# Kernel optimization log

Hardware: AMD Instinct MI355X
Metric: run time of the kernel (lower is better)

The kernel has to match this reference:

```python
import jax, jax.numpy as jnp
import numpy as np

N_NODES = 100000
N_EDGES = 3200000
N_GRAPHS = 512
DIM_H = 128
N_LAYERS = 3
N_CLASSES = 10
BN_EPS = 1e-5


def setup_inputs() -> dict:
    key = jax.random.key(0)
    ks = jax.random.split(key, 16)
    s = 1.0 / np.sqrt(DIM_H)
    x = jax.random.normal(ks[0], (N_NODES, DIM_H), dtype=jnp.float32)
    edge_index = jax.random.randint(ks[1], (2, N_EDGES), 0, N_NODES, dtype=jnp.int64)
    batch = jnp.sort(jax.random.randint(ks[2], (N_NODES,), 0, N_GRAPHS, dtype=jnp.int64))
    W1 = jax.random.uniform(ks[3], (N_LAYERS, DIM_H, DIM_H), jnp.float32, -s, s)
    b1 = jax.random.uniform(ks[4], (N_LAYERS, DIM_H), jnp.float32, -s, s)
    gamma = jnp.ones((N_LAYERS, DIM_H), jnp.float32)
    beta = jnp.zeros((N_LAYERS, DIM_H), jnp.float32)
    rmean = 0.1 * jax.random.normal(ks[5], (N_LAYERS, DIM_H), dtype=jnp.float32)
    rvar = jax.random.uniform(ks[6], (N_LAYERS, DIM_H), jnp.float32, 0.5, 1.5)
    W2 = jax.random.uniform(ks[7], (N_LAYERS, DIM_H, DIM_H), jnp.float32, -s, s)
    b2 = jax.random.uniform(ks[8], (N_LAYERS, DIM_H), jnp.float32, -s, s)
    dcat = DIM_H * N_LAYERS
    sf = 1.0 / np.sqrt(dcat)
    Wfin = jax.random.uniform(ks[9], (dcat, dcat), jnp.float32, -sf, sf)
    bfin = jax.random.uniform(ks[10], (dcat,), jnp.float32, -sf, sf)
    Wout = jax.random.uniform(ks[11], (dcat, N_CLASSES), jnp.float32, -sf, sf)
    bout = jax.random.uniform(ks[12], (N_CLASSES,), jnp.float32, -sf, sf)
    return {"x": x, "edge_index": edge_index, "batch": batch, "num_layers": N_LAYERS,
            "W1": W1, "b1": b1, "gamma": gamma, "beta": beta, "rmean": rmean, "rvar": rvar,
            "W2": W2, "b2": b2, "Wfin": Wfin, "bfin": bfin, "Wout": Wout, "bout": bout}


def reference(x, edge_index, batch, num_layers, W1, b1, gamma, beta, rmean, rvar, W2, b2, Wfin, bfin, Wout, bout):
    src, dst = edge_index[0], edge_index[1]
    h = x
    pooled = []
    for i in range(num_layers):
        # GINConv (eps=0): MLP(x + sum_{j in N(i)} x_j)
        aggr = jax.ops.segment_sum(h[src], dst, num_segments=N_NODES)
        z = (h + aggr) @ W1[i] + b1[i]
        # BatchNorm1d in eval mode (running stats)
        z = gamma[i] * (z - rmean[i]) * jax.lax.rsqrt(rvar[i] + BN_EPS) + beta[i]
        z = jax.nn.relu(z)
        h = jax.nn.relu(z @ W2[i] + b2[i])
        # global_add_pool: segment-sum over graph ids
        pooled.append(jax.ops.segment_sum(h, batch, num_segments=N_GRAPHS))
    h_fin = jnp.concatenate(pooled, axis=1)  # [G, dim_h*num_layers]
    h_fin = jax.nn.relu(h_fin @ Wfin + bfin)
    # dropout p=0.5 is identity in eval mode
    logits = h_fin @ Wout + bout
    return logits, jax.nn.log_softmax(logits, axis=1)
```

## Files before the change

### kernel.cpp

```cpp
#include <hip/hip_runtime.h>
#include <stdint.h>

#define N_NODES 100000
#define N_EDGES 3200000
#define N_GRAPHS 512
#define DIM 128
#define M_PAD 100096
#define NGB (M_PAD / 256)
#define NBUCK 391
#define CAP 9216
#define TILE 4096
#define NTILE 782
#define XMM_NB 392

typedef __bf16 bf16x8 __attribute__((ext_vector_type(8)));
typedef float f32x4 __attribute__((ext_vector_type(4)));

__device__ __forceinline__ unsigned short f2bf(float f) {
  unsigned u = __float_as_uint(f);
  u = u + 0x7FFFu + ((u >> 16) & 1u);
  return (unsigned short)(u >> 16);
}
__device__ __forceinline__ float bflo(unsigned v) { return __uint_as_float(v << 16); }
__device__ __forceinline__ float bfhi(unsigned v) { return __uint_as_float(v & 0xFFFF0000u); }
__device__ __forceinline__ float bfs(unsigned short v) { return __uint_as_float(((unsigned)v) << 16); }
__device__ __forceinline__ unsigned packbf(float a, float b) {
  return (unsigned)f2bf(a) | ((unsigned)f2bf(b) << 16);
}

__global__ void k_zero32(int* __restrict__ p, int n) {
  int i = blockIdx.x * 256 + threadIdx.x;
  if (i < n) p[i] = 0;
}

__global__ __launch_bounds__(256) void k_bucket(const int* __restrict__ ei,
                                                int* __restrict__ cnt,
                                                unsigned* __restrict__ rec) {
  __shared__ int hist[NBUCK];
  __shared__ int curs[NBUCK];
  int t = threadIdx.x;
  int base_e = blockIdx.x * TILE;
  int es[16], ed[16];
#pragma unroll
  for (int k = 0; k < 16; ++k) {
    int e = base_e + k * 256 + t;
    if (e < N_EDGES) { es[k] = ei[e]; ed[k] = ei[N_EDGES + e]; }
    else ed[k] = -1;
  }
  for (int i = t; i < NBUCK; i += 256) hist[i] = 0;
  __syncthreads();
#pragma unroll
  for (int k = 0; k < 16; ++k)
    if (ed[k] >= 0) atomicAdd(&hist[ed[k] >> 8], 1);
  __syncthreads();
  for (int i = t; i < NBUCK; i += 256) {
    int h = hist[i];
    int g = h ? atomicAdd(&cnt[i], h) : 0;
    curs[i] = i * CAP + g;
  }
  __syncthreads();
#pragma unroll
  for (int k = 0; k < 16; ++k) {
    if (ed[k] >= 0) {
      int b = ed[k] >> 8;
      int pos = atomicAdd(&curs[b], 1);
      rec[pos] = ((unsigned)es[k] << 8) | (unsigned)(ed[k] & 255);
    }
  }
}

__global__ __launch_bounds__(512) void k_bscan(const int* __restrict__ cnt,
                                               int* __restrict__ bbase,
                                               int* __restrict__ row_ptr) {
  __shared__ int sc[512];
  int t = threadIdx.x;
  int tot = (t < NBUCK) ? min(cnt[t], CAP) : 0;
  sc[t] = tot; __syncthreads();
  for (int off = 1; off < 512; off <<= 1) {
    int x = (t >= off) ? sc[t - off] : 0;
    __syncthreads();
    sc[t] += x;
    __syncthreads();
  }
  if (t < NBUCK) bbase[t] = sc[t] - tot;
  if (t == NBUCK - 1) {
    bbase[NBUCK] = sc[t];
    row_ptr[N_NODES] = sc[t];
  }
}

__global__ __launch_bounds__(256) void k_build(const unsigned* __restrict__ rec,
                                               const int* __restrict__ cnt,
                                               const int* __restrict__ bbase,
                                               int* __restrict__ row_ptr,
                                               int* __restrict__ col) {
  __shared__ int hist[256];
  __shared__ int sc[256];
  __shared__ int curs[256];
  int b = blockIdx.x, t = threadIdx.x;
  int n = min(cnt[b], CAP);
  const unsigned* p = rec + (size_t)b * CAP;
  hist[t] = 0; __syncthreads();
  for (int i = t; i < n; i += 256) atomicAdd(&hist[p[i] & 255u], 1);
  __syncthreads();
  int v = hist[t];
  sc[t] = v; __syncthreads();
  for (int off = 1; off < 256; off <<= 1) {
    int x = (t >= off) ? sc[t - off] : 0;
    __syncthreads();
    sc[t] += x;
    __syncthreads();
  }
  int excl = bbase[b] + sc[t] - v;
  int node = (b << 8) + t;
  if (node < N_NODES) row_ptr[node] = excl;
  curs[t] = excl;
  __syncthreads();
  for (int i = t; i < n; i += 256) {
    unsigned w = p[i];
    int pos = atomicAdd(&curs[w & 255u], 1);
    col[pos] = (int)(w >> 8);
  }
}

__global__ __launch_bounds__(256) void k_xmm1(const float* __restrict__ x,
                                              float* __restrict__ pmax,
                                              float* __restrict__ pmin) {
  __shared__ float smx[8][32][4];
  __shared__ float smn[8][32][4];
  int t = threadIdx.x;
  int c4 = t & 31;
  int ro = t >> 5;
  float mx0 = 0.f, mx1 = 0.f, mx2 = 0.f, mx3 = 0.f;
  float mn0 = 0.f, mn1 = 0.f, mn2 = 0.f, mn3 = 0.f;
  for (int row = blockIdx.x * 8 + ro; row < N_NODES; row += XMM_NB * 8) {
    float4 v = ((const float4*)x)[(size_t)row * 32 + c4];
    mx0 = fmaxf(mx0, v.x); mn0 = fmaxf(mn0, -v.x);
    mx1 = fmaxf(mx1, v.y); mn1 = fmaxf(mn1, -v.y);
    mx2 = fmaxf(mx2, v.z); mn2 = fmaxf(mn2, -v.z);
    mx3 = fmaxf(mx3, v.w); mn3 = fmaxf(mn3, -v.w);
  }
  smx[ro][c4][0] = mx0; smx[ro][c4][1] = mx1; smx[ro][c4][2] = mx2; smx[ro][c4][3] = mx3;
  smn[ro][c4][0] = mn0; smn[ro][c4][1] = mn1; smn[ro][c4][2] = mn2; smn[ro][c4][3] = mn3;
  __syncthreads();
  for (int off = 4; off > 0; off >>= 1) {
    if (ro < off) {
#pragma unroll
      for (int k = 0; k < 4; ++k) {
        smx[ro][c4][k] = fmaxf(smx[ro][c4][k], smx[ro + off][c4][k]);
        smn[ro][c4][k] = fmaxf(smn[ro][c4][k], smn[ro + off][c4][k]);
      }
    }
    __syncthreads();
  }
  if (ro == 0) {
#pragma unroll
    for (int k = 0; k < 4; ++k) {
      pmax[blockIdx.x * 128 + c4 * 4 + k] = smx[0][c4][k];
      pmin[blockIdx.x * 128 + c4 * 4 + k] = smn[0][c4][k];
    }
  }
}

__global__ __launch_bounds__(64) void k_xmm2(const float* __restrict__ pmax,
                                             const float* __restrict__ pmin,
                                             float* __restrict__ xmx,
                                             float* __restrict__ xminf) {
  int c = blockIdx.x & 127;
  int isMin = blockIdx.x >> 7;
  const float* src = isMin ? pmin : pmax;
  int l = threadIdx.x;
  float m = 0.f;
  for (int p2 = l; p2 < XMM_NB; p2 += 64) m = fmaxf(m, src[p2 * 128 + c]);
#pragma unroll
  for (int off = 32; off > 0; off >>= 1) m = fmaxf(m, __shfl_down(m, off));
  if (l == 0) {
    if (isMin) xminf[c] = -m;
    else xmx[c] = m;
  }
}

__global__ __launch_bounds__(64) void k_hred(const float* __restrict__ pmaxb,
                                             float* __restrict__ hmax) {
  int c = blockIdx.x;
  float m = 0.f;
  for (int b = threadIdx.x; b < NGB; b += 64) m = fmaxf(m, pmaxb[(size_t)b * 128 + c]);
#pragma unroll
  for (int off = 32; off > 0; off >>= 1) m = fmaxf(m, __shfl_down(m, off));
  if (threadIdx.x == 0) hmax[c] = m;
}

__global__ void k_convx(const float* __restrict__ x, const float* __restrict__ qmin,
                        const float* __restrict__ qmax, unsigned short* __restrict__ xq) {
  int i = blockIdx.x * 256 + threadIdx.x;
  if (i >= M_PAD * 64) return;
  int lane = i & 63;
  unsigned short o = 0;
  if ((i >> 6) < N_NODES) {
    float mn0 = qmin[2 * lane], mn1 = qmin[2 * lane + 1];
    float r0 = qmax[2 * lane] - mn0, r1 = qmax[2 * lane + 1] - mn1;
    float is0 = r0 > 1e-20f ? 255.f / r0 : 0.f;
    float is1 = r1 > 1e-20f ? 255.f / r1 : 0.f;
    float2 f = ((const float2*)x)[i];
    int q0 = (int)rintf((f.x - mn0) * is0); q0 = min(max(q0, 0), 255);
    int q1 = (int)rintf((f.y - mn1) * is1); q1 = min(max(q1, 0), 255);
    o = (unsigned short)(q0 | (q1 << 8));
  }
  xq[i] = o;
}

__global__ void k_quant(const unsigned* __restrict__ hbf, const float* __restrict__ qmax,
                        unsigned short* __restrict__ hq) {
  int i = blockIdx.x * 256 + threadIdx.x;
  if (i >= M_PAD * 64) return;
  if ((i >> 6) >= N_NODES) { hq[i] = 0; return; }
  int lane = i & 63;
  float mx0 = qmax[2 * lane], mx1 = qmax[2 * lane + 1];
  float is0 = mx0 > 1e-20f ? 255.f / mx0 : 0.f;
  float is1 = mx1 > 1e-20f ? 255.f / mx1 : 0.f;
  unsigned v = hbf[i];
  int q0 = (int)rintf(bflo(v) * is0); q0 = min(max(q0, 0), 255);
  int q1 = (int)rintf(bfhi(v) * is1); q1 = min(max(q1, 0), 255);
  hq[i] = (unsigned short)(q0 | (q1 << 8));
}

__global__ void k_convw(const float* __restrict__ W1, const float* __restrict__ W2,
                        unsigned short* __restrict__ Wt1, unsigned short* __restrict__ Wt2) {
  int i = blockIdx.x * 256 + threadIdx.x;
  if (i >= 3 * DIM * DIM) return;
  int l = i >> 14, rem = i & 16383, k = rem >> 7, n = rem & 127;
  int o = (l << 14) + (n << 7) + k;
  Wt1[o] = f2bf(W1[i]);
  Wt2[o] = f2bf(W2[i]);
}

__global__ void k_coef(const float* __restrict__ b1, const float* __restrict__ gamma,
                       const float* __restrict__ beta, const float* __restrict__ rmean,
                       const float* __restrict__ rvar, const float* __restrict__ b2,
                       float* __restrict__ sA1, float* __restrict__ sB1,
                       float* __restrict__ sA2, float* __restrict__ sB2) {
  int i = blockIdx.x * 128 + threadIdx.x;
  if (i >= 3 * DIM) return;
  float sa = gamma[i] * rsqrtf(rvar[i] + 1e-5f);
  sA1[i] = sa;
  sB1[i] = fmaf(sa, b1[i] - rmean[i], beta[i]);
  sA2[i] = 1.0f;
  sB2[i] = b2[i];
}

__global__ __launch_bounds__(256) void k_aggr(const unsigned short* __restrict__ hq,
                                              const int* __restrict__ row_ptr,
                                              const int* __restrict__ col,
                                              const float* __restrict__ qmin,
                                              const float* __restrict__ qmax,
                                              unsigned* __restrict__ tmp) {
  const uint4* hq128 = (const uint4*)hq;
  const unsigned* hq32 = (const unsigned*)hq;
  int wv = (blockIdx.x << 2) + (threadIdx.x >> 6);
  int lane = threadIdx.x & 63;
  int grp = lane >> 3;
  int lo8 = lane & 7;
  int dw = lane & 31;
  if (wv >= M_PAD) return;
  if (wv >= N_NODES) {
    ((uint2*)(tmp + (size_t)wv * 64))[dw] = make_uint2(0u, 0u);
    return;
  }
  unsigned ae0 = 0, ae1 = 0, ae2 = 0, ae3 = 0;
  unsigned ao0 = 0, ao1 = 0, ao2 = 0, ao3 = 0;
  int s = __builtin_amdgcn_readfirstlane(row_ptr[wv]);
  int e = __builtin_amdgcn_readfirstlane(row_ptr[wv + 1]);
  int pidx = (lo8 << 3) + grp;
  for (int base = s; base < e; base += 32) {
    int n = e - base; if (n > 32) n = 32;
    int cv = (pidx < n) ? col[base + pidx] : 0;
    int s0 = __builtin_amdgcn_ds_swizzle(cv, 0x18);
    int s1 = __builtin_amdgcn_ds_swizzle(cv, 0x38);
    int s2 = __builtin_amdgcn_ds_swizzle(cv, 0x58);
    int s3 = __builtin_amdgcn_ds_swizzle(cv, 0x78);
    s0 = (grp      < n) ? s0 : N_NODES;
    s1 = (grp +  8 < n) ? s1 : N_NODES;
    s2 = (grp + 16 < n) ? s2 : N_NODES;
    s3 = (grp + 24 < n) ? s3 : N_NODES;
    uint4 v0 = hq128[s0 * 8 + lo8];
    uint4 v1 = hq128[s1 * 8 + lo8];
    uint4 v2 = hq128[s2 * 8 + lo8];
    uint4 v3 = hq128[s3 * 8 + lo8];
    ae0 += v0.x & 0x00FF00FFu; ao0 += (v0.x >> 8) & 0x00FF00FFu;
    ae1 += v0.y & 0x00FF00FFu; ao1 += (v0.y >> 8) & 0x00FF00FFu;
    ae2 += v0.z & 0x00FF00FFu; ao2 += (v0.z >> 8) & 0x00FF00FFu;
    ae3 += v0.w & 0x00FF00FFu; ao3 += (v0.w >> 8) & 0x00FF00FFu;
    ae0 += v1.x & 0x00FF00FFu; ao0 += (v1.x >> 8) & 0x00FF00FFu;
    ae1 += v1.y & 0x00FF00FFu; ao1 += (v1.y >> 8) & 0x00FF00FFu;
    ae2 += v1.z & 0x00FF00FFu; ao2 += (v1.z >> 8) & 0x00FF00FFu;
    ae3 += v1.w & 0x00FF00FFu; ao3 += (v1.w >> 8) & 0x00FF00FFu;
    ae0 += v2.x & 0x00FF00FFu; ao0 += (v2.x >> 8) & 0x00FF00FFu;
    ae1 += v2.y & 0x00FF00FFu; ao1 += (v2.y >> 8) & 0x00FF00FFu;
    ae2 += v2.z & 0x00FF00FFu; ao2 += (v2.z >> 8) & 0x00FF00FFu;
    ae3 += v2.w & 0x00FF00FFu; ao3 += (v2.w >> 8) & 0x00FF00FFu;
    ae0 += v3.x & 0x00FF00FFu; ao0 += (v3.x >> 8) & 0x00FF00FFu;
    ae1 += v3.y & 0x00FF00FFu; ao1 += (v3.y >> 8) & 0x00FF00FFu;
    ae2 += v3.z & 0x00FF00FFu; ao2 += (v3.z >> 8) & 0x00FF00FFu;
    ae3 += v3.w & 0x00FF00FFu; ao3 += (v3.w >> 8) & 0x00FF00FFu;
  }
  ae0 += __shfl_xor(ae0, 8); ae0 += __shfl_xor(ae0, 16); ae0 += __shfl_xor(ae0, 32);
  ae1 += __shfl_xor(ae1, 8); ae1 += __shfl_xor(ae1, 16); ae1 += __shfl_xor(ae1, 32);
  ae2 += __shfl_xor(ae2, 8); ae2 += __shfl_xor(ae2, 16); ae2 += __shfl_xor(ae2, 32);
  ae3 += __shfl_xor(ae3, 8); ae3 += __shfl_xor(ae3, 16); ae3 += __shfl_xor(ae3, 32);
  ao0 += __shfl_xor(ao0, 8); ao0 += __shfl_xor(ao0, 16); ao0 += __shfl_xor(ao0, 32);
  ao1 += __shfl_xor(ao1, 8); ao1 += __shfl_xor(ao1, 16); ao1 += __shfl_xor(ao1, 32);
  ao2 += __shfl_xor(ao2, 8); ao2 += __shfl_xor(ao2, 16); ao2 += __shfl_xor(ao2, 32);
  ao3 += __shfl_xor(ao3, 8); ao3 += __shfl_xor(ao3, 16); ao3 += __shfl_xor(ao3, 32);
  {
    int ba = ((dw >> 2) & 7) << 2;
    unsigned f0 = (unsigned)__builtin_amdgcn_ds_bpermute(ba, (int)ae0);
    unsigned f1 = (unsigned)__builtin_amdgcn_ds_bpermute(ba, (int)ae1);
    unsigned f2 = (unsigned)__builtin_amdgcn_ds_bpermute(ba, (int)ae2);
    unsigned f3 = (unsigned)__builtin_amdgcn_ds_bpermute(ba, (int)ae3);
    unsigned g0 = (unsigned)__builtin_amdgcn_ds_bpermute(ba, (int)ao0);
    unsigned g1 = (unsigned)__builtin_amdgcn_ds_bpermute(ba, (int)ao1);
    unsigned g2 = (unsigned)__builtin_amdgcn_ds_bpermute(ba, (int)ao2);
    unsigned g3 = (unsigned)__builtin_amdgcn_ds_bpermute(ba, (int)ao3);
    unsigned el = (dw & 1) ? f1 : f0;
    unsigned eh = (dw & 1) ? f3 : f2;
    unsigned ae = (dw & 2) ? eh : el;
    unsigned ol = (dw & 1) ? g1 : g0;
    unsigned oh = (dw & 1) ? g3 : g2;
    unsigned ao = (dw & 2) ? oh : ol;
    if (lane < 32) {
      unsigned v = hq32[wv * 32 + dw];
      ae += v & 0x00FF00FFu;
      ao += (v >> 8) & 0x00FF00FFu;
      float cntf = (float)(e - s + 1);
      float4 qn = ((const float4*)qmin)[dw];
      float4 qx = ((const float4*)qmax)[dw];
      const float k255 = 1.0f / 255.0f;
      float A0 = fmaf(qn.x, cntf, (qx.x - qn.x) * k255 * (float)(ae & 0xFFFFu));
      float A1 = fmaf(qn.y, cntf, (qx.y - qn.y) * k255 * (float)(ao & 0xFFFFu));
      float A2 = fmaf(qn.z, cntf, (qx.z - qn.z) * k255 * (float)(ae >> 16));
      float A3 = fmaf(qn.w, cntf, (qx.w - qn.w) * k255 * (float)(ao >> 16));
      ((uint2*)(tmp + (size_t)wv * 64))[dw] = make_uint2(packbf(A0, A1), packbf(A2, A3));
    }
  }
}

__global__ __launch_bounds__(256, 2) void k_gemm12(const unsigned short* __restrict__ A,
                                                   const unsigned short* __restrict__ Wt1,
                                                   const float* __restrict__ sA1,
                                                   const float* __restrict__ sB1,
                                                   const unsigned short* __restrict__ Wt2,
                                                   const float* __restrict__ sA2,
                                                   const float* __restrict__ sB2,
                                                   const int* __restrict__ batch,
                                                   unsigned short* __restrict__ out,
                                                   float* __restrict__ pooled8, int layer,
                                                   float* __restrict__ pmaxb, int do_max) {
  __shared__ unsigned short zt[4][64][136];
  __shared__ float colred[128];
  __shared__ int sgid[256];
  int w = threadIdx.x >> 6, lane = threadIdx.x & 63;
  int q = lane >> 4, n16 = lane & 15;
  int rbase = (blockIdx.x << 8) + (w << 6);
  if (do_max && threadIdx.x < 128) colred[threadIdx.x] = 0.f;
  {
    int rr = (blockIdx.x << 8) + threadIdx.x;
    sgid[threadIdx.x] = (rr < N_NODES) ? batch[rr] : -1;
  }

  {
    bf16x8 Bf[4][8];
#pragma unroll
    for (int ks = 0; ks < 4; ++ks)
#pragma unroll
      for (int c = 0; c < 8; ++c)
        Bf[ks][c] = *(const bf16x8*)(Wt1 + (size_t)((c << 4) + n16) * DIM + ks * 32 + q * 8);
#pragma unroll
    for (int t = 0; t < 4; ++t) {
      int r0 = rbase + (t << 4);
      f32x4 acc[8] = {};
#pragma unroll
      for (int ks = 0; ks < 4; ++ks) {
        bf16x8 a = *(const bf16x8*)(A + (size_t)(r0 + n16) * DIM + ks * 32 + q * 8);
#pragma unroll
        for (int c = 0; c < 8; ++c)
          acc[c] = __builtin_amdgcn_mfma_f32_16x16x32_bf16(a, Bf[ks][c], acc[c], 0, 0, 0);
      }
#pragma unroll
      for (int c = 0; c < 8; ++c) {
        int colc = (c << 4) + n16;
        float s = sA1[colc], tt = sB1[colc];
#pragma unroll
        for (int r = 0; r < 4; ++r) {
          float v = fmaxf(fmaf(s, acc[c][r], tt), 0.0f);
          zt[w][(t << 4) + (q << 2) + r][colc] = f2bf(v);
        }
      }
    }
  }

  float mcol[8];
#pragma unroll
  for (int c = 0; c < 8; ++c) mcol[c] = 0.f;
  {
    bf16x8 Bf[4][8];
#pragma unroll
    for (int ks = 0; ks < 4; ++ks)
#pragma unroll
      for (int c = 0; c < 8; ++c)
        Bf[ks][c] = *(const bf16x8*)(Wt2 + (size_t)((c << 4) + n16) * DIM + ks * 32 + q * 8);
#pragma unroll
    for (int t = 0; t < 4; ++t) {
      int r0 = rbase + (t << 4);
      f32x4 acc[8] = {};
#pragma unroll
      for (int ks = 0; ks < 4; ++ks) {
        bf16x8 a = *(const bf16x8*)(&zt[w][(t << 4) + n16][ks * 32 + q * 8]);
#pragma unroll
        for (int c = 0; c < 8; ++c)
          acc[c] = __builtin_amdgcn_mfma_f32_16x16x32_bf16(a, Bf[ks][c], acc[c], 0, 0, 0);
      }
      __builtin_amdgcn_s_waitcnt(0);
#pragma unroll
      for (int c = 0; c < 8; ++c) {
        int colc = (c << 4) + n16;
        float s = sA2[colc], tt = sB2[colc];
#pragma unroll
        for (int r = 0; r < 4; ++r) {
          float v = fmaxf(fmaf(s, acc[c][r], tt), 0.0f);
          mcol[c] = fmaxf(mcol[c], v);
          unsigned short hv = f2bf(v);
          out[(size_t)(r0 + (q << 2) + r) * DIM + colc] = hv;
          zt[w][(t << 4) + (q << 2) + r][colc] = hv;
        }
      }
    }
  }
  __syncthreads();

  {
    const unsigned short* ztf = &zt[0][0][0];
    int colp = threadIdx.x & 127, grp = threadIdx.x >> 7;
    int cp = blockIdx.x & 7;
    float pacc = 0.f;
    int gcur = sgid[grp << 7];
    for (int r = 0; r < 128; ++r) {
      int row = (grp << 7) + r;
      int g = sgid[row];
      if (g != gcur) {
        if (gcur >= 0)
          atomicAdd(&pooled8[((size_t)cp * N_GRAPHS + gcur) * 384 + layer * DIM + colp], pacc);
        pacc = 0.f; gcur = g;
      }
      if (g >= 0) pacc += bfs(ztf[row * 136 + colp]);
    }
    if (gcur >= 0)
      atomicAdd(&pooled8[((size_t)cp * N_GRAPHS + gcur) * 384 + layer * DIM + colp], pacc);
  }

  if (do_max) {
#pragma unroll
    for (int c = 0; c < 8; ++c)
      atomicMax((int*)&colred[(c << 4) + n16], __float_as_int(mcol[c]));
    __syncthreads();
    if (threadIdx.x < 128)
      pmaxb[(size_t)blockIdx.x * 128 + threadIdx.x] = colred[threadIdx.x];
  }
}

__global__ __launch_bounds__(384) void k_head(const float* __restrict__ pooled8,
                                              const float* __restrict__ Wfin,
                                              const float* __restrict__ bfin,
                                              const float* __restrict__ Wout,
                                              const float* __restrict__ bout,
                                              float* __restrict__ out) {
  __shared__ float p[8][384];
  __shared__ float hf[8][392];
  __shared__ float lg[8][10];
  __shared__ float lse[8];
  int t = threadIdx.x, g0 = blockIdx.x << 3;
  for (int i = t; i < 8 * 384; i += 384) {
    int gl = i / 384, k = i % 384;
    float s = 0.f;
#pragma unroll
    for (int cp = 0; cp < 8; ++cp)
      s += pooled8[((size_t)cp * N_GRAPHS + g0 + gl) * 384 + k];
    p[gl][k] = s;
  }
  __syncthreads();
  float bb = bfin[t];
  float acc[8];
#pragma unroll
  for (int g = 0; g < 8; ++g) acc[g] = bb;
  for (int k = 0; k < 384; ++k) {
    float wv = Wfin[k * 384 + t];
#pragma unroll
    for (int g = 0; g < 8; ++g) acc[g] = fmaf(p[g][k], wv, acc[g]);
  }
#pragma unroll
  for (int g = 0; g < 8; ++g) hf[g][t] = fmaxf(acc[g], 0.f);
  __syncthreads();
  if (t < 80) {
    int g = t / 10, c = t % 10;
    float a = bout[c];
    for (int k = 0; k < 384; ++k) a = fmaf(hf[g][k], Wout[k * 10 + c], a);
    lg[g][c] = a;
  }
  __syncthreads();
  if (t < 8) {
    float m = lg[t][0];
#pragma unroll
    for (int i = 1; i < 10; ++i) m = fmaxf(m, lg[t][i]);
    float ss = 0.f;
#pragma unroll
    for (int i = 0; i < 10; ++i) ss += __expf(lg[t][i] - m);
    lse[t] = m + __logf(ss);
  }
  __syncthreads();
  if (t < 80) {
    int g = t / 10, c = t % 10;
    out[(size_t)(g0 + g) * 10 + c] = lg[g][c];
    out[(size_t)N_GRAPHS * 10 + (size_t)(g0 + g) * 10 + c] = lg[g][c] - lse[g];
  }
}

extern "C" void kernel_launch(void* const* d_in, const int* in_sizes, int n_in,
                              void* d_out, int out_size, void* d_ws, size_t ws_size,
                              hipStream_t stream) {
  const float* x     = (const float*)d_in[0];
  const int*   ei    = (const int*)d_in[1];
  const int*   batch = (const int*)d_in[2];
  const float* W1    = (const float*)d_in[4];
  const float* b1    = (const float*)d_in[5];
  const float* gamma = (const float*)d_in[6];
  const float* beta  = (const float*)d_in[7];
  const float* rmean = (const float*)d_in[8];
  const float* rvar  = (const float*)d_in[9];
  const float* W2    = (const float*)d_in[10];
  const float* b2    = (const float*)d_in[11];
  const float* Wfin  = (const float*)d_in[12];
  const float* bfin  = (const float*)d_in[13];
  const float* Wout  = (const float*)d_in[14];
  const float* bout  = (const float*)d_in[15];
  float* out = (float*)d_out;

  char* p = (char*)d_ws;
  auto alloc = [&](size_t bytes) { char* r = p; p += (bytes + 255) & ~255ull; return r; };
  int* cnt      = (int*)alloc(NBUCK * 4);
  unsigned* rec = (unsigned*)alloc((size_t)NBUCK * CAP * 4);
  int* bbase    = (int*)alloc((NBUCK + 1) * 4);
  int* row_ptr  = (int*)alloc((N_NODES + 1) * 4);
  int* colb     = (int*)alloc((size_t)N_EDGES * 4);
  unsigned short* xq  = (unsigned short*)alloc((size_t)M_PAD * 64 * 2);
  unsigned short* hqb = (unsigned short*)alloc((size_t)M_PAD * 64 * 2);
  unsigned* hbf  = (unsigned*)alloc((size_t)M_PAD * 64 * 4);
  unsigned* tmpb = (unsigned*)alloc((size_t)M_PAD * 64 * 4);
  unsigned short* Wt1 = (unsigned short*)alloc(3 * DIM * DIM * 2);
  unsigned short* Wt2 = (unsigned short*)alloc(3 * DIM * DIM * 2);
  float* pmax   = (float*)alloc((size_t)XMM_NB * 128 * 4);
  float* pmin   = (float*)alloc((size_t)XMM_NB * 128 * 4);
  float* pmaxb  = (float*)alloc((size_t)NGB * 128 * 4);
  float* sA1    = (float*)alloc(384 * 4);
  float* sB1    = (float*)alloc(384 * 4);
  float* sA2    = (float*)alloc(384 * 4);
  float* sB2    = (float*)alloc(384 * 4);
  float* qbuf   = (float*)alloc(1024 * 4);
  float* xmx    = qbuf + 128;
  float* xminf  = qbuf + 256;
  float* hmax0  = qbuf + 384;
  float* hmax1  = qbuf + 512;
  float* zeros  = qbuf + 640;
  float* pooled8 = (float*)alloc((size_t)8 * N_GRAPHS * 384 * 4);

  k_zero32<<<(NBUCK + 255) / 256, 256, 0, stream>>>(cnt, NBUCK);
  k_zero32<<<4, 256, 0, stream>>>((int*)qbuf, 1024);
  k_zero32<<<(8 * N_GRAPHS * 384 + 255) / 256, 256, 0, stream>>>((int*)pooled8, 8 * N_GRAPHS * 384);

  k_bucket<<<NTILE, 256, 0, stream>>>(ei, cnt, rec);
  k_bscan<<<1, 512, 0, stream>>>(cnt, bbase, row_ptr);
  k_build<<<NBUCK, 256, 0, stream>>>(rec, cnt, bbase, row_ptr, colb);

  k_xmm1<<<XMM_NB, 256, 0, stream>>>(x, pmax, pmin);
  k_xmm2<<<256, 64, 0, stream>>>(pmax, pmin, xmx, xminf);
  k_convx<<<(M_PAD * 64 + 255) / 256, 256, 0, stream>>>(x, xminf, xmx, xq);
  k_convw<<<(3 * DIM * DIM + 255) / 256, 256, 0, stream>>>(W1, W2, Wt1, Wt2);
  k_coef<<<3, 128, 0, stream>>>(b1, gamma, beta, rmean, rvar, b2, sA1, sB1, sA2, sB2);

  k_aggr<<<M_PAD / 4, 256, 0, stream>>>(xq, row_ptr, colb, xminf, xmx, tmpb);
  k_gemm12<<<NGB, 256, 0, stream>>>((const unsigned short*)tmpb, Wt1, sA1, sB1,
                                    Wt2, sA2, sB2, batch, (unsigned short*)hbf,
                                    pooled8, 0, pmaxb, 1);
  k_hred<<<128, 64, 0, stream>>>(pmaxb, hmax0);
  k_quant<<<(M_PAD * 64 + 255) / 256, 256, 0, stream>>>(hbf, hmax0, hqb);
  k_aggr<<<M_PAD / 4, 256, 0, stream>>>(hqb, row_ptr, colb, zeros, hmax0, tmpb);
  k_gemm12<<<NGB, 256, 0, stream>>>((const unsigned short*)tmpb, Wt1 + DIM * DIM,
                                    sA1 + DIM, sB1 + DIM, Wt2 + DIM * DIM,
                                    sA2 + DIM, sB2 + DIM, batch, (unsigned short*)hbf,
                                    pooled8, 1, pmaxb, 1);
  k_hred<<<128, 64, 0, stream>>>(pmaxb, hmax1);
  k_quant<<<(M_PAD * 64 + 255) / 256, 256, 0, stream>>>(hbf, hmax1, hqb);
  k_aggr<<<M_PAD / 4, 256, 0, stream>>>(hqb, row_ptr, colb, zeros, hmax1, tmpb);
  k_gemm12<<<NGB, 256, 0, stream>>>((const unsigned short*)tmpb, Wt1 + 2 * DIM * DIM,
                                    sA1 + 2 * DIM, sB1 + 2 * DIM, Wt2 + 2 * DIM * DIM,
                                    sA2 + 2 * DIM, sB2 + 2 * DIM, batch, (unsigned short*)hbf,
                                    pooled8, 2, pmaxb, 0);

  k_head<<<N_GRAPHS / 8, 384, 0, stream>>>(pooled8, Wfin, bfin, Wout, bout, out);
}
```

Before: 621.1 us.

## Process two nodes per wavefront in aggregation with batched gathers

```diff
diff --git a/kernel.cpp b/kernel.cpp
--- a/kernel.cpp
+++ b/kernel.cpp
@@ -248,6 +248,63 @@
   sB2[i] = b2[i];
 }
 
+#define SWZ(cv, J) __builtin_amdgcn_ds_swizzle((cv), (0x18 | ((J) << 5)))
+
+__device__ __forceinline__ void acc8(const uint4& v, unsigned& e0, unsigned& e1,
+                                     unsigned& e2, unsigned& e3, unsigned& o0,
+                                     unsigned& o1, unsigned& o2, unsigned& o3) {
+  e0 += v.x & 0x00FF00FFu; o0 += (v.x >> 8) & 0x00FF00FFu;
+  e1 += v.y & 0x00FF00FFu; o1 += (v.y >> 8) & 0x00FF00FFu;
+  e2 += v.z & 0x00FF00FFu; o2 += (v.z >> 8) & 0x00FF00FFu;
+  e3 += v.w & 0x00FF00FFu; o3 += (v.w >> 8) & 0x00FF00FFu;
+}
+
+__device__ __forceinline__ void epi_store(unsigned ae0, unsigned ae1, unsigned ae2, unsigned ae3,
+                                          unsigned ao0, unsigned ao1, unsigned ao2, unsigned ao3,
+                                          int wv, int s, int e, int lane, int dw,
+                                          const unsigned* __restrict__ hq32,
+                                          const float* __restrict__ qmin,
+                                          const float* __restrict__ qmax,
+                                          unsigned* __restrict__ tmp) {
+  ae0 += __shfl_xor(ae0, 8); ae0 += __shfl_xor(ae0, 16); ae0 += __shfl_xor(ae0, 32);
+  ae1 += __shfl_xor(ae1, 8); ae1 += __shfl_xor(ae1, 16); ae1 += __shfl_xor(ae1, 32);
+  ae2 += __shfl_xor(ae2, 8); ae2 += __shfl_xor(ae2, 16); ae2 += __shfl_xor(ae2, 32);
+  ae3 += __shfl_xor(ae3, 8); ae3 += __shfl_xor(ae3, 16); ae3 += __shfl_xor(ae3, 32);
+  ao0 += __shfl_xor(ao0, 8); ao0 += __shfl_xor(ao0, 16); ao0 += __shfl_xor(ao0, 32);
+  ao1 += __shfl_xor(ao1, 8); ao1 += __shfl_xor(ao1, 16); ao1 += __shfl_xor(ao1, 32);
+  ao2 += __shfl_xor(ao2, 8); ao2 += __shfl_xor(ao2, 16); ao2 += __shfl_xor(ao2, 32);
+  ao3 += __shfl_xor(ao3, 8); ao3 += __shfl_xor(ao3, 16); ao3 += __shfl_xor(ao3, 32);
+  int ba = ((dw >> 2) & 7) << 2;
+  unsigned f0 = (unsigned)__builtin_amdgcn_ds_bpermute(ba, (int)ae0);
+  unsigned f1 = (unsigned)__builtin_amdgcn_ds_bpermute(ba, (int)ae1);
+  unsigned f2 = (unsigned)__builtin_amdgcn_ds_bpermute(ba, (int)ae2);
+  unsigned f3 = (unsigned)__builtin_amdgcn_ds_bpermute(ba, (int)ae3);
+  unsigned g0 = (unsigned)__builtin_amdgcn_ds_bpermute(ba, (int)ao0);
+  unsigned g1 = (unsigned)__builtin_amdgcn_ds_bpermute(ba, (int)ao1);
+  unsigned g2 = (unsigned)__builtin_amdgcn_ds_bpermute(ba, (int)ao2);
+  unsigned g3 = (unsigned)__builtin_amdgcn_ds_bpermute(ba, (int)ao3);
+  unsigned el = (dw & 1) ? f1 : f0;
+  unsigned eh = (dw & 1) ? f3 : f2;
+  unsigned ae = (dw & 2) ? eh : el;
+  unsigned ol = (dw & 1) ? g1 : g0;
+  unsigned oh = (dw & 1) ? g3 : g2;
+  unsigned ao = (dw & 2) ? oh : ol;
+  if (lane < 32) {
+    unsigned v = hq32[wv * 32 + dw];
+    ae += v & 0x00FF00FFu;
+    ao += (v >> 8) & 0x00FF00FFu;
+    float cntf = (float)(e - s + 1);
+    float4 qn = ((const float4*)qmin)[dw];
+    float4 qx = ((const float4*)qmax)[dw];
+    const float k255 = 1.0f / 255.0f;
+    float A0 = fmaf(qn.x, cntf, (qx.x - qn.x) * k255 * (float)(ae & 0xFFFFu));
+    float A1 = fmaf(qn.y, cntf, (qx.y - qn.y) * k255 * (float)(ao & 0xFFFFu));
+    float A2 = fmaf(qn.z, cntf, (qx.z - qn.z) * k255 * (float)(ae >> 16));
+    float A3 = fmaf(qn.w, cntf, (qx.w - qn.w) * k255 * (float)(ao >> 16));
+    ((uint2*)(tmp + (size_t)wv * 64))[dw] = make_uint2(packbf(A0, A1), packbf(A2, A3));
+  }
+}
+
 __global__ __launch_bounds__(256) void k_aggr(const unsigned short* __restrict__ hq,
                                               const int* __restrict__ row_ptr,
                                               const int* __restrict__ col,
@@ -256,92 +313,125 @@
                                               unsigned* __restrict__ tmp) {
   const uint4* hq128 = (const uint4*)hq;
   const unsigned* hq32 = (const unsigned*)hq;
-  int wv = (blockIdx.x << 2) + (threadIdx.x >> 6);
+  int wid = (blockIdx.x << 2) + (threadIdx.x >> 6);
+  int wv0 = wid << 1, wv1 = wv0 + 1;
   int lane = threadIdx.x & 63;
   int grp = lane >> 3;
   int lo8 = lane & 7;
   int dw = lane & 31;
-  if (wv >= M_PAD) return;
-  if (wv >= N_NODES) {
-    ((uint2*)(tmp + (size_t)wv * 64))[dw] = make_uint2(0u, 0u);
+  if (wv0 >= M_PAD) return;
+  if (wv0 >= N_NODES) {
+    ((uint2*)(tmp + (size_t)wv0 * 64))[dw] = make_uint2(0u, 0u);
+    if (wv1 < M_PAD) ((uint2*)(tmp + (size_t)wv1 * 64))[dw] = make_uint2(0u, 0u);
     return;
   }
-  unsigned ae0 = 0, ae1 = 0, ae2 = 0, ae3 = 0;
-  unsigned ao0 = 0, ao1 = 0, ao2 = 0, ao3 = 0;
-  int s = __builtin_amdgcn_readfirstlane(row_ptr[wv]);
-  int e = __builtin_amdgcn_readfirstlane(row_ptr[wv + 1]);
+  int s0 = __builtin_amdgcn_readfirstlane(row_ptr[wv0]);
+  int mB = __builtin_amdgcn_readfirstlane(row_ptr[wv0 + 1]);
+  int e1 = __builtin_amdgcn_readfirstlane(row_ptr[wv0 + 2]);
+  int nA = mB - s0; if (nA > 64) nA = 64;
+  int nB = e1 - mB; if (nB > 64) nB = 64;
   int pidx = (lo8 << 3) + grp;
-  for (int base = s; base < e; base += 32) {
-    int n = e - base; if (n > 32) n = 32;
+  int cvA = (pidx < nA) ? col[s0 + pidx] : 0;
+  int cvB = (pidx < nB) ? col[mB + pidx] : 0;
+
+  unsigned ae0 = 0, ae1 = 0, ae2 = 0, ae3 = 0, ao0 = 0, ao1 = 0, ao2 = 0, ao3 = 0;
+  unsigned be0 = 0, be1 = 0, be2 = 0, be3 = 0, bo0 = 0, bo1 = 0, bo2 = 0, bo3 = 0;
+
+  int a0 = SWZ(cvA, 0); a0 = (grp      < nA) ? a0 : N_NODES;
+  int a1 = SWZ(cvA, 1); a1 = (grp +  8 < nA) ? a1 : N_NODES;
+  int a2 = SWZ(cvA, 2); a2 = (grp + 16 < nA) ? a2 : N_NODES;
+  int a3 = SWZ(cvA, 3); a3 = (grp + 24 < nA) ? a3 : N_NODES;
+  uint4 vA0 = hq128[(size_t)a0 * 8 + lo8];
+  uint4 vA1 = hq128[(size_t)a1 * 8 + lo8];
+  uint4 vA2 = hq128[(size_t)a2 * 8 + lo8];
+  uint4 vA3 = hq128[(size_t)a3 * 8 + lo8];
+  int b0 = SWZ(cvB, 0); b0 = (grp      < nB) ? b0 : N_NODES;
+  int b1 = SWZ(cvB, 1); b1 = (grp +  8 < nB) ? b1 : N_NODES;
+  int b2 = SWZ(cvB, 2); b2 = (grp + 16 < nB) ? b2 : N_NODES;
+  int b3 = SWZ(cvB, 3); b3 = (grp + 24 < nB) ? b3 : N_NODES;
+  uint4 vB0 = hq128[(size_t)b0 * 8 + lo8];
+  uint4 vB1 = hq128[(size_t)b1 * 8 + lo8];
+  uint4 vB2 = hq128[(size_t)b2 * 8 + lo8];
+  uint4 vB3 = hq128[(size_t)b3 * 8 + lo8];
+
+  bool hA = nA > 32, hB = nB > 32;
+  uint4 vA4, vA5, vA6, vA7, vB4, vB5, vB6, vB7;
+  if (hA) {
+    int a4 = SWZ(cvA, 4); a4 = (grp + 32 < nA) ? a4 : N_NODES;
+    int a5 = SWZ(cvA, 5); a5 = (grp + 40 < nA) ? a5 : N_NODES;
+    int a6 = SWZ(cvA, 6); a6 = (grp + 48 < nA) ? a6 : N_NODES;
+    int a7 = SWZ(cvA, 7); a7 = (grp + 56 < nA) ? a7 : N_NODES;
+    vA4 = hq128[(size_t)a4 * 8 + lo8];
+    vA5 = hq128[(size_t)a5 * 8 + lo8];
+    vA6 = hq128[(size_t)a6 * 8 + lo8];
+    vA7 = hq128[(size_t)a7 * 8 + lo8];
+  }
+  acc8(vA0, ae0, ae1, ae2, ae3, ao0, ao1, ao2, ao3);
+  acc8(vA1, ae0, ae1, ae2, ae3, ao0, ao1, ao2, ao3);
+  acc8(vA2, ae0, ae1, ae2, ae3, ao0, ao1, ao2, ao3);
+  acc8(vA3, ae0, ae1, ae2, ae3, ao0, ao1, ao2, ao3);
+  if (hB) {
+    int b4 = SWZ(cvB, 4); b4 = (grp + 32 < nB) ? b4 : N_NODES;
+    int b5 = SWZ(cvB, 5); b5 = (grp + 40 < nB) ? b5 : N_NODES;
+    int b6 = SWZ(cvB, 6); b6 = (grp + 48 < nB) ? b6 : N_NODES;
+    int b7 = SWZ(cvB, 7); b7 = (grp + 56 < nB) ? b7 : N_NODES;
+    vB4 = hq128[(size_t)b4 * 8 + lo8];
+    vB5 = hq128[(size_t)b5 * 8 + lo8];
+    vB6 = hq128[(size_t)b6 * 8 + lo8];
+    vB7 = hq128[(size_t)b7 * 8 + lo8];
+  }
+  acc8(vB0, be0, be1, be2, be3, bo0, bo1, bo2, bo3);
+  acc8(vB1, be0, be1, be2, be3, bo0, bo1, bo2, bo3);
+  acc8(vB2, be0, be1, be2, be3, bo0, bo1, bo2, bo3);
+  acc8(vB3, be0, be1, be2, be3, bo0, bo1, bo2, bo3);
+  if (hA) {
+    acc8(vA4, ae0, ae1, ae2, ae3, ao0, ao1, ao2, ao3);
+    acc8(vA5, ae0, ae1, ae2, ae3, ao0, ao1, ao2, ao3);
+    acc8(vA6, ae0, ae1, ae2, ae3, ao0, ao1, ao2, ao3);
+    acc8(vA7, ae0, ae1, ae2, ae3, ao0, ao1, ao2, ao3);
+  }
+  if (hB) {
+    acc8(vB4, be0, be1, be2, be3, bo0, bo1, bo2, bo3);
+    acc8(vB5, be0, be1, be2, be3, bo0, bo1, bo2, bo3);
+    acc8(vB6, be0, be1, be2, be3, bo0, bo1, bo2, bo3);
+    acc8(vB7, be0, be1, be2, be3, bo0, bo1, bo2, bo3);
+  }
+
+  for (int base = s0 + 64; base < mB; base += 32) {
+    int n = mB - base; if (n > 32) n = 32;
     int cv = (pidx < n) ? col[base + pidx] : 0;
-    int s0 = __builtin_amdgcn_ds_swizzle(cv, 0x18);
-    int s1 = __builtin_amdgcn_ds_swizzle(cv, 0x38);
-    int s2 = __builtin_amdgcn_ds_swizzle(cv, 0x58);
-    int s3 = __builtin_amdgcn_ds_swizzle(cv, 0x78);
-    s0 = (grp      < n) ? s0 : N_NODES;
-    s1 = (grp +  8 < n) ? s1 : N_NODES;
-    s2 = (grp + 16 < n) ? s2 : N_NODES;
-    s3 = (grp + 24 < n) ? s3 : N_NODES;
-    uint4 v0 = hq128[s0 * 8 + lo8];
-    uint4 v1 = hq128[s1 * 8 + lo8];
-    uint4 v2 = hq128[s2 * 8 + lo8];
-    uint4 v3 = hq128[s3 * 8 + lo8];
-    ae0 += v0.x & 0x00FF00FFu; ao0 += (v0.x >> 8) & 0x00FF00FFu;
-    ae1 += v0.y & 0x00FF00FFu; ao1 += (v0.y >> 8) & 0x00FF00FFu;
-    ae2 += v0.z & 0x00FF00FFu; ao2 += (v0.z >> 8) & 0x00FF00FFu;
-    ae3 += v0.w & 0x00FF00FFu; ao3 += (v0.w >> 8) & 0x00FF00FFu;
-    ae0 += v1.x & 0x00FF00FFu; ao0 += (v1.x >> 8) & 0x00FF00FFu;
-    ae1 += v1.y & 0x00FF00FFu; ao1 += (v1.y >> 8) & 0x00FF00FFu;
-    ae2 += v1.z & 0x00FF00FFu; ao2 += (v1.z >> 8) & 0x00FF00FFu;
-    ae3 += v1.w & 0x00FF00FFu; ao3 += (v1.w >> 8) & 0x00FF00FFu;
-    ae0 += v2.x & 0x00FF00FFu; ao0 += (v2.x >> 8) & 0x00FF00FFu;
-    ae1 += v2.y & 0x00FF00FFu; ao1 += (v2.y >> 8) & 0x00FF00FFu;
-    ae2 += v2.z & 0x00FF00FFu; ao2 += (v2.z >> 8) & 0x00FF00FFu;
-    ae3 += v2.w & 0x00FF00FFu; ao3 += (v2.w >> 8) & 0x00FF00FFu;
-    ae0 += v3.x & 0x00FF00FFu; ao0 += (v3.x >> 8) & 0x00FF00FFu;
-    ae1 += v3.y & 0x00FF00FFu; ao1 += (v3.y >> 8) & 0x00FF00FFu;
-    ae2 += v3.z & 0x00FF00FFu; ao2 += (v3.z >> 8) & 0x00FF00FFu;
-    ae3 += v3.w & 0x00FF00FFu; ao3 += (v3.w >> 8) & 0x00FF00FFu;
-  }
-  ae0 += __shfl_xor(ae0, 8); ae0 += __shfl_xor(ae0, 16); ae0 += __shfl_xor(ae0, 32);
-  ae1 += __shfl_xor(ae1, 8); ae1 += __shfl_xor(ae1, 16); ae1 += __shfl_xor(ae1, 32);
-  ae2 += __shfl_xor(ae2, 8); ae2 += __shfl_xor(ae2, 16); ae2 += __shfl_xor(ae2, 32);
-  ae3 += __shfl_xor(ae3, 8); ae3 += __shfl_xor(ae3, 16); ae3 += __shfl_xor(ae3, 32);
-  ao0 += __shfl_xor(ao0, 8); ao0 += __shfl_xor(ao0, 16); ao0 += __shfl_xor(ao0, 32);
-  ao1 += __shfl_xor(ao1, 8); ao1 += __shfl_xor(ao1, 16); ao1 += __shfl_xor(ao1, 32);
-  ao2 += __shfl_xor(ao2, 8); ao2 += __shfl_xor(ao2, 16); ao2 += __shfl_xor(ao2, 32);
-  ao3 += __shfl_xor(ao3, 8); ao3 += __shfl_xor(ao3, 16); ao3 += __shfl_xor(ao3, 32);
-  {
-    int ba = ((dw >> 2) & 7) << 2;
-    unsigned f0 = (unsigned)__builtin_amdgcn_ds_bpermute(ba, (int)ae0);
-    unsigned f1 = (unsigned)__builtin_amdgcn_ds_bpermute(ba, (int)ae1);
-    unsigned f2 = (unsigned)__builtin_amdgcn_ds_bpermute(ba, (int)ae2);
-    unsigned f3 = (unsigned)__builtin_amdgcn_ds_bpermute(ba, (int)ae3);
-    unsigned g0 = (unsigned)__builtin_amdgcn_ds_bpermute(ba, (int)ao0);
-    unsigned g1 = (unsigned)__builtin_amdgcn_ds_bpermute(ba, (int)ao1);
-    unsigned g2 = (unsigned)__builtin_amdgcn_ds_bpermute(ba, (int)ao2);
-    unsigned g3 = (unsigned)__builtin_amdgcn_ds_bpermute(ba, (int)ao3);
-    unsigned el = (dw & 1) ? f1 : f0;
-    unsigned eh = (dw & 1) ? f3 : f2;
-    unsigned ae = (dw & 2) ? eh : el;
-    unsigned ol = (dw & 1) ? g1 : g0;
-    unsigned oh = (dw & 1) ? g3 : g2;
-    unsigned ao = (dw & 2) ? oh : ol;
-    if (lane < 32) {
-      unsigned v = hq32[wv * 32 + dw];
-      ae += v & 0x00FF00FFu;
-      ao += (v >> 8) & 0x00FF00FFu;
-      float cntf = (float)(e - s + 1);
-      float4 qn = ((const float4*)qmin)[dw];
-      float4 qx = ((const float4*)qmax)[dw];
-      const float k255 = 1.0f / 255.0f;
-      float A0 = fmaf(qn.x, cntf, (qx.x - qn.x) * k255 * (float)(ae & 0xFFFFu));
-      float A1 = fmaf(qn.y, cntf, (qx.y - qn.y) * k255 * (float)(ao & 0xFFFFu));
-      float A2 = fmaf(qn.z, cntf, (qx.z - qn.z) * k255 * (float)(ae >> 16));
-      float A3 = fmaf(qn.w, cntf, (qx.w - qn.w) * k255 * (float)(ao >> 16));
-      ((uint2*)(tmp + (size_t)wv * 64))[dw] = make_uint2(packbf(A0, A1), packbf(A2, A3));
-    }
-  }
+    int t0 = SWZ(cv, 0); t0 = (grp      < n) ? t0 : N_NODES;
+    int t1 = SWZ(cv, 1); t1 = (grp +  8 < n) ? t1 : N_NODES;
+    int t2 = SWZ(cv, 2); t2 = (grp + 16 < n) ? t2 : N_NODES;
+    int t3 = SWZ(cv, 3); t3 = (grp + 24 < n) ? t3 : N_NODES;
+    uint4 u0 = hq128[(size_t)t0 * 8 + lo8];
+    uint4 u1 = hq128[(size_t)t1 * 8 + lo8];
+    uint4 u2 = hq128[(size_t)t2 * 8 + lo8];
+    uint4 u3 = hq128[(size_t)t3 * 8 + lo8];
+    acc8(u0, ae0, ae1, ae2, ae3, ao0, ao1, ao2, ao3);
+    acc8(u1, ae0, ae1, ae2, ae3, ao0, ao1, ao2, ao3);
+    acc8(u2, ae0, ae1, ae2, ae3, ao0, ao1, ao2, ao3);
+    acc8(u3, ae0, ae1, ae2, ae3, ao0, ao1, ao2, ao3);
+  }
+  for (int base = mB + 64; base < e1; base += 32) {
+    int n = e1 - base; if (n > 32) n = 32;
+    int cv = (pidx < n) ? col[base + pidx] : 0;
+    int t0 = SWZ(cv, 0); t0 = (grp      < n) ? t0 : N_NODES;
+    int t1 = SWZ(cv, 1); t1 = (grp +  8 < n) ? t1 : N_NODES;
+    int t2 = SWZ(cv, 2); t2 = (grp + 16 < n) ? t2 : N_NODES;
+    int t3 = SWZ(cv, 3); t3 = (grp + 24 < n) ? t3 : N_NODES;
+    uint4 u0 = hq128[(size_t)t0 * 8 + lo8];
+    uint4 u1 = hq128[(size_t)t1 * 8 + lo8];
+    uint4 u2 = hq128[(size_t)t2 * 8 + lo8];
+    uint4 u3 = hq128[(size_t)t3 * 8 + lo8];
+    acc8(u0, be0, be1, be2, be3, bo0, bo1, bo2, bo3);
+    acc8(u1, be0, be1, be2, be3, bo0, bo1, bo2, bo3);
+    acc8(u2, be0, be1, be2, be3, bo0, bo1, bo2, bo3);
+    acc8(u3, be0, be1, be2, be3, bo0, bo1, bo2, bo3);
+  }
+
+  epi_store(ae0, ae1, ae2, ae3, ao0, ao1, ao2, ao3, wv0, s0, mB, lane, dw, hq32, qmin, qmax, tmp);
+  epi_store(be0, be1, be2, be3, bo0, bo1, bo2, bo3, wv1, mB, e1, lane, dw, hq32, qmin, qmax, tmp);
 }
 
 __global__ __launch_bounds__(256, 2) void k_gemm12(const unsigned short* __restrict__ A,
@@ -585,20 +675,20 @@
   k_convw<<<(3 * DIM * DIM + 255) / 256, 256, 0, stream>>>(W1, W2, Wt1, Wt2);
   k_coef<<<3, 128, 0, stream>>>(b1, gamma, beta, rmean, rvar, b2, sA1, sB1, sA2, sB2);
 
-  k_aggr<<<M_PAD / 4, 256, 0, stream>>>(xq, row_ptr, colb, xminf, xmx, tmpb);
+  k_aggr<<<M_PAD / 8, 256, 0, stream>>>(xq, row_ptr, colb, xminf, xmx, tmpb);
   k_gemm12<<<NGB, 256, 0, stream>>>((const unsigned short*)tmpb, Wt1, sA1, sB1,
                                     Wt2, sA2, sB2, batch, (unsigned short*)hbf,
                                     pooled8, 0, pmaxb, 1);
   k_hred<<<128, 64, 0, stream>>>(pmaxb, hmax0);
   k_quant<<<(M_PAD * 64 + 255) / 256, 256, 0, stream>>>(hbf, hmax0, hqb);
-  k_aggr<<<M_PAD / 4, 256, 0, stream>>>(hqb, row_ptr, colb, zeros, hmax0, tmpb);
+  k_aggr<<<M_PAD / 8, 256, 0, stream>>>(hqb, row_ptr, colb, zeros, hmax0, tmpb);
   k_gemm12<<<NGB, 256, 0, stream>>>((const unsigned short*)tmpb, Wt1 + DIM * DIM,
                                     sA1 + DIM, sB1 + DIM, Wt2 + DIM * DIM,
                                     sA2 + DIM, sB2 + DIM, batch, (unsigned short*)hbf,
                                     pooled8, 1, pmaxb, 1);
   k_hred<<<128, 64, 0, stream>>>(pmaxb, hmax1);
   k_quant<<<(M_PAD * 64 + 255) / 256, 256, 0, stream>>>(hbf, hmax1, hqb);
-  k_aggr<<<M_PAD / 4, 256, 0, stream>>>(hqb, row_ptr, colb, zeros, hmax1, tmpb);
+  k_aggr<<<M_PAD / 8, 256, 0, stream>>>(hqb, row_ptr, colb, zeros, hmax1, tmpb);
   k_gemm12<<<NGB, 256, 0, stream>>>((const unsigned short*)tmpb, Wt1 + 2 * DIM * DIM,
                                     sA1 + 2 * DIM, sB1 + 2 * DIM, Wt2 + 2 * DIM * DIM,
                                     sA2 + 2 * DIM, sB2 + 2 * DIM, batch, (unsigned short*)hbf,
```

New measurement: 624.4 us. Within noise of the previous version (+0.5%).
